# Optimization experiments

Measured on AMD Instinct MI355X. Metric: run time of the kernel, lower is better.

Reference implementation:

```python
import jax, jax.numpy as jnp
import numpy as np

SCALE = 100.0

def square_distance(src, dst):
    # src: [B,N,D], dst: [B,M,D] -> [B,N,M] squared euclidean distances
    d = -2.0 * jnp.einsum('bnd,bmd->bnm', src, dst)
    d = d + jnp.sum(src * src, axis=-1)[:, :, None]
    d = d + jnp.sum(dst * dst, axis=-1)[:, None, :]
    return d

def setup_inputs() -> dict:
    key = jax.random.key(0)
    k1, k2 = jax.random.split(key)
    B, N, M, D = 8, 8192, 8192, 3
    pred = jax.random.normal(k1, (B, N, D), dtype=jnp.float32)
    gt = jax.random.normal(k2, (B, M, D), dtype=jnp.float32)
    return {"pred": pred, "gt": gt}

def reference(pred, gt):
    dis = square_distance(pred, gt)              # [B,N,M]
    pred_to_gt = jnp.min(dis, axis=2).mean(axis=1)  # [B]
    gt_to_pred = jnp.min(dis, axis=1).mean(axis=1)  # [B]
    return (0.5 * pred_to_gt + 0.5 * gt_to_pred).mean() * SCALE
```

## Files before the change

kernel.cpp:

```cpp
#include <hip/hip_runtime.h>


#define B_DIM 8
#define N_DIM 8192
#define MT    (N_DIM / 32)
#define BLOCK 256
#define PPW   4

typedef short  bf16x8 __attribute__((ext_vector_type(8)));
typedef float  f32x16 __attribute__((ext_vector_type(16)));

__device__ __forceinline__ unsigned short bf16_rne(float f) {
    unsigned int u = __float_as_uint(f);
    u += 0x7fffu + ((u >> 16) & 1u);
    return (unsigned short)(u >> 16);
}
__device__ __forceinline__ float bf16f(unsigned short h) {
    return __uint_as_float(((unsigned int)h) << 16);
}

__global__ __launch_bounds__(256) void chamfer_prep(
    const float* __restrict__ pred, const float* __restrict__ gt,
    unsigned short* __restrict__ bpack, float* __restrict__ out)
{
    const int i   = blockIdx.x * 256 + threadIdx.x;
    if (i == 0) out[0] = 0.0f;
    const int dir = i >> 16;
    const int bm  = i & 0xFFFF;
    const float* dst = dir ? pred : gt;
    const float x = dst[3*bm+0], y = dst[3*bm+1], z = dst[3*bm+2];
    const unsigned short hx = bf16_rne(x), hy = bf16_rne(y), hz = bf16_rne(z);
    const unsigned short lx = bf16_rne(x - bf16f(hx));
    const unsigned short ly = bf16_rne(y - bf16f(hy));
    const unsigned short lz = bf16_rne(z - bf16f(hz));
    const float gn = x*x + y*y + z*z;
    const unsigned short gnh = bf16_rne(gn), gnl = bf16_rne(gn - bf16f(gnh));
    const unsigned short one = 0x3F80;

    const int b  = bm >> 13, m = bm & (N_DIM - 1);
    const int mt = m >> 5,   c = m & 31;
    const int dirb = (dir << 3) | b;
    unsigned short* p0 = bpack + ((size_t)(dirb * MT + mt) * 64 + c) * 8;
    unsigned short* p1 = p0 + 32 * 8;
    bf16x8 h0 = {(short)hx,(short)hy,(short)hz,(short)lx,(short)ly,(short)lz,(short)hx,(short)hy};
    bf16x8 h1 = {(short)hz,(short)one,(short)one,(short)gnh,(short)gnl,0,0,0};
    *(bf16x8*)p0 = h0;
    *(bf16x8*)p1 = h1;
}

__global__ __launch_bounds__(BLOCK, 2) void chamfer_partial(
    const float* __restrict__ pred, const float* __restrict__ gt,
    const bf16x8* __restrict__ bpack, float* __restrict__ out)
{
    __shared__ float cbuf[PPW * 16 * 128];
    __shared__ float wsum[2];
    const int dirb = blockIdx.x;
    const int dir  = dirb >> 3, b = dirb & 7;
    const int w    = threadIdx.x >> 6, lane = threadIdx.x & 63;
    const int halfk = lane >> 5,  col = lane & 31;
    const int nsub = w & 1;
    const int mh   = w >> 1;

    const float* src  = dir ? gt : pred;
    const float* srcb = src + (size_t)b * N_DIM * 3;

    bf16x8 afrag[PPW];
    #pragma unroll
    for (int p = 0; p < PPW; ++p) {
        const int ntile = blockIdx.y * 8 + nsub * PPW + p;
        const int n = ntile * 32 + col;
        const float x = srcb[3*n+0], y = srcb[3*n+1], z = srcb[3*n+2];
        const float ax = -2.f*x, ay = -2.f*y, az = -2.f*z;
        const unsigned short ahx = bf16_rne(ax), ahy = bf16_rne(ay), ahz = bf16_rne(az);
        const unsigned short alx = bf16_rne(ax - bf16f(ahx));
        const unsigned short aly = bf16_rne(ay - bf16f(ahy));
        const unsigned short alz = bf16_rne(az - bf16f(ahz));
        const float pn = x*x + y*y + z*z;
        const unsigned short pnh = bf16_rne(pn), pnl = bf16_rne(pn - bf16f(pnh));
        const unsigned short one = 0x3F80;
        bf16x8 a0 = {(short)ahx,(short)ahy,(short)ahz,(short)ahx,(short)ahy,(short)ahz,(short)alx,(short)aly};
        bf16x8 a1 = {(short)alz,(short)pnh,(short)pnl,(short)one,(short)one,0,0,0};
        afrag[p] = (halfk == 0) ? a0 : a1;
    }

    float best[PPW][16];
    #pragma unroll
    for (int p = 0; p < PPW; ++p)
        #pragma unroll
        for (int r = 0; r < 16; ++r) best[p][r] = 1e30f;

    const bf16x8* bw = bpack + (size_t)dirb * (MT * 64) + (size_t)(mh * 128) * 64 + lane;

#define FOLD(c0_, c1_) { \
        _Pragma("unroll") \
        for (int p = 0; p < PPW; ++p) { \
            f32x16 d0, d1; \
            asm volatile( \
                "v_mfma_f32_32x32x16_bf16 %0, %2, %3, 0\n\t" \
                "v_mfma_f32_32x32x16_bf16 %1, %2, %4, 0\n\t" \
                "s_nop 7\n\t" \
                "s_nop 3" \
                : "=&v"(d0), "=&v"(d1) \
                : "v"(afrag[p]), "v"(c0_), "v"(c1_)); \
            __builtin_amdgcn_sched_barrier(0x34); \
            _Pragma("unroll") \
            for (int r = 0; r < 16; ++r) \
                asm("v_min3_f32 %0, %0, %1, %2" \
                    : "+v"(best[p][r]) : "v"(d0[r]), "v"(d1[r])); \
        } \
    }

    bf16x8 cA0 = bw[0],   cA1 = bw[64];
    bf16x8 cB0 = bw[128], cB1 = bw[192];
    bf16x8 cC0 = bw[256], cC1 = bw[320];
    bf16x8 cD0 = bw[384], cD1 = bw[448];
    bw += 512;
    for (int t = 0; t < 15; ++t) {
        FOLD(cA0, cA1);  cA0 = bw[0];   cA1 = bw[64];
        FOLD(cB0, cB1);  cB0 = bw[128]; cB1 = bw[192];
        FOLD(cC0, cC1);  cC0 = bw[256]; cC1 = bw[320];
        FOLD(cD0, cD1);  cD0 = bw[384]; cD1 = bw[448];
        bw += 512;
    }
    FOLD(cA0, cA1);
    FOLD(cB0, cB1);
    FOLD(cC0, cC1);
    FOLD(cD0, cD1);

    if (mh == 1) {
        #pragma unroll
        for (int p = 0; p < PPW; ++p)
            #pragma unroll
            for (int r = 0; r < 16; ++r)
                cbuf[(p * 16 + r) * 128 + nsub * 64 + lane] = best[p][r];
    }
    __syncthreads();
    if (mh == 0) {
        float bsum = 0.f;
        #pragma unroll
        for (int p = 0; p < PPW; ++p) {
            float s = 0.f;
            #pragma unroll
            for (int r = 0; r < 16; ++r) {
                float v = fminf(best[p][r], cbuf[(p * 16 + r) * 128 + nsub * 64 + lane]);
                v = fminf(v, __shfl_xor(v, 1,  64));
                v = fminf(v, __shfl_xor(v, 2,  64));
                v = fminf(v, __shfl_xor(v, 4,  64));
                v = fminf(v, __shfl_xor(v, 8,  64));
                v = fminf(v, __shfl_xor(v, 16, 64));
                s += v;
            }
            bsum += s + __shfl_xor(s, 32, 64);
        }
        if (lane == 0) wsum[nsub] = bsum;
    }
    __syncthreads();
    if (threadIdx.x == 0) {
        const float scale = 100.0f * 0.5f / ((float)B_DIM * (float)N_DIM);
        atomicAdd(out, (wsum[0] + wsum[1]) * scale);
    }
}

extern "C" void kernel_launch(void* const* d_in, const int* in_sizes, int n_in,
                              void* d_out, int out_size, void* d_ws, size_t ws_size,
                              hipStream_t stream) {
    const float* pred = (const float*)d_in[0];
    const float* gt   = (const float*)d_in[1];
    float* out = (float*)d_out;
    unsigned short* bpack = (unsigned short*)d_ws;

    chamfer_prep<<<(2 * B_DIM * N_DIM) / 256, 256, 0, stream>>>(pred, gt, bpack, out);

    dim3 grid(16, N_DIM / 256);
    chamfer_partial<<<grid, BLOCK, 0, stream>>>(pred, gt, (const bf16x8*)bpack, out);
}
```

Measured before the change: 92.76 us.

## Compute distance matrix once and derive both chamfer directions from it

Instead of running the MFMA distance sweep separately for pred→gt and gt→pred, a single pass computes pred×gt tiles. It keeps row minima in registers and also reduces column minima per 32-row tile, writing them to a workspace buffer. A third kernel min-reduces these column partials across the 64 row blocks and sums them. This halves the matrix-core work, but adds extra VALU min ops per tile, a 16MB partial write/read and a third kernel launch. It falls back to the old two-direction path when the workspace is too small.

```diff
diff --git a/kernel.cpp b/kernel.cpp
--- a/kernel.cpp
+++ b/kernel.cpp
@@ -19,7 +19,184 @@
     return __uint_as_float(((unsigned int)h) << 16);
 }
 
-__global__ __launch_bounds__(256) void chamfer_prep(
+__global__ __launch_bounds__(256) void prep_gt(
+    const float* __restrict__ gt, unsigned short* __restrict__ gtpack,
+    float* __restrict__ out)
+{
+    const int i = blockIdx.x * 256 + threadIdx.x;
+    if (i == 0) out[0] = 0.0f;
+    const float x = gt[3*i+0], y = gt[3*i+1], z = gt[3*i+2];
+    const unsigned short hx = bf16_rne(x), hy = bf16_rne(y), hz = bf16_rne(z);
+    const unsigned short lx = bf16_rne(x - bf16f(hx));
+    const unsigned short ly = bf16_rne(y - bf16f(hy));
+    const unsigned short lz = bf16_rne(z - bf16f(hz));
+    const float gn = x*x + y*y + z*z;
+    const unsigned short gnh = bf16_rne(gn), gnl = bf16_rne(gn - bf16f(gnh));
+    const unsigned short one = 0x3F80;
+
+    const int b  = i >> 13, m = i & (N_DIM - 1);
+    const int mt = m >> 5,  c = m & 31;
+    unsigned short* p0 = gtpack + ((size_t)(b * MT + mt) * 64 + c) * 8;
+    unsigned short* p1 = p0 + 32 * 8;
+    bf16x8 h0 = {(short)hx,(short)hy,(short)hz,(short)lx,(short)ly,(short)lz,(short)hx,(short)hy};
+    bf16x8 h1 = {(short)hz,(short)one,(short)one,(short)gnh,(short)gnl,0,0,0};
+    *(bf16x8*)p0 = h0;
+    *(bf16x8*)p1 = h1;
+}
+
+__global__ __launch_bounds__(BLOCK, 2) void chamfer_main(
+    const float* __restrict__ pred, const bf16x8* __restrict__ gtpack,
+    float* __restrict__ colpart, float* __restrict__ out)
+{
+    __shared__ float cbuf[3 * PPW * 16 * 64];
+    const int b    = blockIdx.x;
+    const int yb   = blockIdx.y;
+    const int w    = threadIdx.x >> 6, lane = threadIdx.x & 63;
+    const int halfk = lane >> 5,  col = lane & 31;
+
+    const float* srcb = pred + (size_t)b * N_DIM * 3;
+    bf16x8 afrag[PPW];
+    #pragma unroll
+    for (int p = 0; p < PPW; ++p) {
+        const int n = (blockIdx.y * 4 + p) * 32 + col;
+        const float x = srcb[3*n+0], y = srcb[3*n+1], z = srcb[3*n+2];
+        const float ax = -2.f*x, ay = -2.f*y, az = -2.f*z;
+        const unsigned short ahx = bf16_rne(ax), ahy = bf16_rne(ay), ahz = bf16_rne(az);
+        const unsigned short alx = bf16_rne(ax - bf16f(ahx));
+        const unsigned short aly = bf16_rne(ay - bf16f(ahy));
+        const unsigned short alz = bf16_rne(az - bf16f(ahz));
+        const float pn = x*x + y*y + z*z;
+        const unsigned short pnh = bf16_rne(pn), pnl = bf16_rne(pn - bf16f(pnh));
+        const unsigned short one = 0x3F80;
+        bf16x8 a0 = {(short)ahx,(short)ahy,(short)ahz,(short)ahx,(short)ahy,(short)ahz,(short)alx,(short)aly};
+        bf16x8 a1 = {(short)alz,(short)pnh,(short)pnl,(short)one,(short)one,0,0,0};
+        afrag[p] = (halfk == 0) ? a0 : a1;
+    }
+
+    float best[PPW][16];
+    #pragma unroll
+    for (int p = 0; p < PPW; ++p)
+        #pragma unroll
+        for (int r = 0; r < 16; ++r) best[p][r] = 1e30f;
+
+    const bf16x8* bw = gtpack + (size_t)b * (MT * 64) + (size_t)(w * 64) * 64 + lane;
+    float* cp = colpart + ((size_t)(b * 64 + yb) * N_DIM) + w * 2048;
+
+#define FOLDC(c0_, c1_) { \
+        float cm0 = 1e30f, cm1 = 1e30f; \
+        _Pragma("unroll") \
+        for (int p = 0; p < PPW; ++p) { \
+            f32x16 d0, d1; \
+            asm volatile( \
+                "v_mfma_f32_32x32x16_bf16 %0, %2, %3, 0\n\t" \
+                "v_mfma_f32_32x32x16_bf16 %1, %2, %4, 0\n\t" \
+                "s_nop 7\n\t" \
+                "s_nop 3" \
+                : "=&v"(d0), "=&v"(d1) \
+                : "v"(afrag[p]), "v"(c0_), "v"(c1_)); \
+            __builtin_amdgcn_sched_barrier(0x34); \
+            _Pragma("unroll") \
+            for (int r = 0; r < 16; ++r) \
+                asm("v_min3_f32 %0, %0, %1, %2" \
+                    : "+v"(best[p][r]) : "v"(d0[r]), "v"(d1[r])); \
+            _Pragma("unroll") \
+            for (int r = 0; r < 16; r += 2) { \
+                asm("v_min3_f32 %0, %0, %1, %2" \
+                    : "+v"(cm0) : "v"(d0[r]), "v"(d0[r+1])); \
+                asm("v_min3_f32 %0, %0, %1, %2" \
+                    : "+v"(cm1) : "v"(d1[r]), "v"(d1[r+1])); \
+            } \
+        } \
+        cm0 = fminf(cm0, __shfl_xor(cm0, 32, 64)); \
+        cm1 = fminf(cm1, __shfl_xor(cm1, 32, 64)); \
+        if (lane < 32) { cp[lane] = cm0; cp[lane + 32] = cm1; } \
+        cp += 64; \
+    }
+
+    bf16x8 cA0 = bw[0],   cA1 = bw[64];
+    bf16x8 cB0 = bw[128], cB1 = bw[192];
+    bf16x8 cC0 = bw[256], cC1 = bw[320];
+    bf16x8 cD0 = bw[384], cD1 = bw[448];
+    bw += 512;
+    for (int t = 0; t < 7; ++t) {
+        FOLDC(cA0, cA1);  cA0 = bw[0];   cA1 = bw[64];
+        FOLDC(cB0, cB1);  cB0 = bw[128]; cB1 = bw[192];
+        FOLDC(cC0, cC1);  cC0 = bw[256]; cC1 = bw[320];
+        FOLDC(cD0, cD1);  cD0 = bw[384]; cD1 = bw[448];
+        bw += 512;
+    }
+    FOLDC(cA0, cA1);
+    FOLDC(cB0, cB1);
+    FOLDC(cC0, cC1);
+    FOLDC(cD0, cD1);
+
+    if (w > 0) {
+        #pragma unroll
+        for (int p = 0; p < PPW; ++p)
+            #pragma unroll
+            for (int r = 0; r < 16; ++r)
+                cbuf[((w - 1) * 64 + p * 16 + r) * 64 + lane] = best[p][r];
+    }
+    __syncthreads();
+    if (w == 0) {
+        float bsum = 0.f;
+        #pragma unroll
+        for (int p = 0; p < PPW; ++p) {
+            float s = 0.f;
+            #pragma unroll
+            for (int r = 0; r < 16; ++r) {
+                float v = best[p][r];
+                v = fminf(v, cbuf[(0 * 64 + p * 16 + r) * 64 + lane]);
+                v = fminf(v, cbuf[(1 * 64 + p * 16 + r) * 64 + lane]);
+                v = fminf(v, cbuf[(2 * 64 + p * 16 + r) * 64 + lane]);
+                v = fminf(v, __shfl_xor(v, 1,  64));
+                v = fminf(v, __shfl_xor(v, 2,  64));
+                v = fminf(v, __shfl_xor(v, 4,  64));
+                v = fminf(v, __shfl_xor(v, 8,  64));
+                v = fminf(v, __shfl_xor(v, 16, 64));
+                s += v;
+            }
+            bsum += s + __shfl_xor(s, 32, 64);
+        }
+        if (lane == 0) {
+            const float scale = 100.0f * 0.5f / ((float)B_DIM * (float)N_DIM);
+            atomicAdd(out, bsum * scale);
+        }
+    }
+}
+
+__global__ __launch_bounds__(256) void chamfer_colreduce(
+    const float* __restrict__ colpart, float* __restrict__ out)
+{
+    const int idx = blockIdx.x * 256 + threadIdx.x;
+    const int b = idx >> 13, m = idx & (N_DIM - 1);
+    const float* base = colpart + (size_t)b * 64 * N_DIM + m;
+    float v0 = 1e30f, v1 = 1e30f, v2 = 1e30f, v3 = 1e30f;
+    #pragma unroll
+    for (int y = 0; y < 64; y += 4) {
+        v0 = fminf(v0, base[(size_t)(y + 0) * N_DIM]);
+        v1 = fminf(v1, base[(size_t)(y + 1) * N_DIM]);
+        v2 = fminf(v2, base[(size_t)(y + 2) * N_DIM]);
+        v3 = fminf(v3, base[(size_t)(y + 3) * N_DIM]);
+    }
+    float v = fminf(fminf(v0, v1), fminf(v2, v3));
+    v += __shfl_xor(v, 1,  64);
+    v += __shfl_xor(v, 2,  64);
+    v += __shfl_xor(v, 4,  64);
+    v += __shfl_xor(v, 8,  64);
+    v += __shfl_xor(v, 16, 64);
+    v += __shfl_xor(v, 32, 64);
+    __shared__ float ws4[4];
+    const int w = threadIdx.x >> 6, lane = threadIdx.x & 63;
+    if (lane == 0) ws4[w] = v;
+    __syncthreads();
+    if (threadIdx.x == 0) {
+        const float scale = 100.0f * 0.5f / ((float)B_DIM * (float)N_DIM);
+        atomicAdd(out, (ws4[0] + ws4[1] + ws4[2] + ws4[3]) * scale);
+    }
+}
+
+__global__ __launch_bounds__(256) void fb_prep(
     const float* __restrict__ pred, const float* __restrict__ gt,
     unsigned short* __restrict__ bpack, float* __restrict__ out)
 {
@@ -36,7 +213,6 @@
     const float gn = x*x + y*y + z*z;
     const unsigned short gnh = bf16_rne(gn), gnl = bf16_rne(gn - bf16f(gnh));
     const unsigned short one = 0x3F80;
-
     const int b  = bm >> 13, m = bm & (N_DIM - 1);
     const int mt = m >> 5,   c = m & 31;
     const int dirb = (dir << 3) | b;
@@ -48,7 +224,7 @@
     *(bf16x8*)p1 = h1;
 }
 
-__global__ __launch_bounds__(BLOCK, 2) void chamfer_partial(
+__global__ __launch_bounds__(BLOCK, 2) void fb_partial(
     const float* __restrict__ pred, const float* __restrict__ gt,
     const bf16x8* __restrict__ bpack, float* __restrict__ out)
 {
@@ -60,15 +236,12 @@
     const int halfk = lane >> 5,  col = lane & 31;
     const int nsub = w & 1;
     const int mh   = w >> 1;
-
     const float* src  = dir ? gt : pred;
     const float* srcb = src + (size_t)b * N_DIM * 3;
-
     bf16x8 afrag[PPW];
     #pragma unroll
     for (int p = 0; p < PPW; ++p) {
-        const int ntile = blockIdx.y * 8 + nsub * PPW + p;
-        const int n = ntile * 32 + col;
+        const int n = (blockIdx.y * 8 + nsub * PPW + p) * 32 + col;
         const float x = srcb[3*n+0], y = srcb[3*n+1], z = srcb[3*n+2];
         const float ax = -2.f*x, ay = -2.f*y, az = -2.f*z;
         const unsigned short ahx = bf16_rne(ax), ahy = bf16_rne(ay), ahz = bf16_rne(az);
@@ -82,15 +255,12 @@
         bf16x8 a1 = {(short)alz,(short)pnh,(short)pnl,(short)one,(short)one,0,0,0};
         afrag[p] = (halfk == 0) ? a0 : a1;
     }
-
     float best[PPW][16];
     #pragma unroll
     for (int p = 0; p < PPW; ++p)
         #pragma unroll
         for (int r = 0; r < 16; ++r) best[p][r] = 1e30f;
-
     const bf16x8* bw = bpack + (size_t)dirb * (MT * 64) + (size_t)(mh * 128) * 64 + lane;
-
 #define FOLD(c0_, c1_) { \
         _Pragma("unroll") \
         for (int p = 0; p < PPW; ++p) { \
@@ -109,7 +279,6 @@
                     : "+v"(best[p][r]) : "v"(d0[r]), "v"(d1[r])); \
         } \
     }
-
     bf16x8 cA0 = bw[0],   cA1 = bw[64];
     bf16x8 cB0 = bw[128], cB1 = bw[192];
     bf16x8 cC0 = bw[256], cC1 = bw[320];
@@ -126,7 +295,6 @@
     FOLD(cB0, cB1);
     FOLD(cC0, cC1);
     FOLD(cD0, cD1);
-
     if (mh == 1) {
         #pragma unroll
         for (int p = 0; p < PPW; ++p)
@@ -167,10 +335,22 @@
     const float* pred = (const float*)d_in[0];
     const float* gt   = (const float*)d_in[1];
     float* out = (float*)d_out;
-    unsigned short* bpack = (unsigned short*)d_ws;
-
-    chamfer_prep<<<(2 * B_DIM * N_DIM) / 256, 256, 0, stream>>>(pred, gt, bpack, out);
-
-    dim3 grid(16, N_DIM / 256);
-    chamfer_partial<<<grid, BLOCK, 0, stream>>>(pred, gt, (const bf16x8*)bpack, out);
-}
+
+    const size_t GT_BYTES  = (size_t)2 << 20;
+    const size_t COL_BYTES = (size_t)B_DIM * 64 * N_DIM * 4;
+
+    if (ws_size >= GT_BYTES + COL_BYTES) {
+        unsigned short* gtpack = (unsigned short*)d_ws;
+        float* colpart = (float*)((char*)d_ws + GT_BYTES);
+        prep_gt<<<(B_DIM * N_DIM) / 256, 256, 0, stream>>>(gt, gtpack, out);
+        dim3 grid(B_DIM, N_DIM / 128);
+        chamfer_main<<<grid, BLOCK, 0, stream>>>(pred, (const bf16x8*)gtpack,
+                                                 colpart, out);
+        chamfer_colreduce<<<(B_DIM * N_DIM) / 256, 256, 0, stream>>>(colpart, out);
+    } else {
+        unsigned short* bpack = (unsigned short*)d_ws;
+        fb_prep<<<(2 * B_DIM * N_DIM) / 256, 256, 0, stream>>>(pred, gt, bpack, out);
+        dim3 grid(16, N_DIM / 256);
+        fb_partial<<<grid, BLOCK, 0, stream>>>(pred, gt, (const bf16x8*)bpack, out);
+    }
+}
```

Measured after the change: 104.0 us. 12.2% more time.
